# Kernel optimization log

Hardware: AMD Instinct MI355X
Metric: run time of the kernel (lower is better)

Reference implementation:

```python
import math
import jax, jax.numpy as jnp
import numpy as np

WS = 4            # window size
LS = 2 * WS       # local context size
NH = 8            # num heads
DIM = 128
EPS = 1e-5


def setup_inputs() -> dict:
    key = jax.random.key(0)
    ks = jax.random.split(key, 8)
    B, C, H, W = 4, DIM, 48, 48
    features = jax.random.normal(ks[0], (B, C, H, W), dtype=jnp.float32)
    s = 0.02
    return {
        'features': features,
        'ln_w': jnp.ones((C,), jnp.float32),
        'ln_b': jnp.zeros((C,), jnp.float32),
        'q_w': jax.random.normal(ks[1], (C, C), jnp.float32) * s,
        'q_b': jnp.zeros((C,), jnp.float32),
        'kv_w': jax.random.normal(ks[2], (2 * C, C), jnp.float32) * s,
        'kv_b': jnp.zeros((2 * C,), jnp.float32),
        'out_w': jax.random.normal(ks[3], (C, C), jnp.float32) * s,
        'out_b': jnp.zeros((C,), jnp.float32),
    }


def _avgpool_tokens(x, k):
    # x: [B,C,H,W] -> [B, (H//k)*(W//k), C]
    B, C, H, W = x.shape
    t = x.reshape(B, C, H // k, k, W // k, k).mean(axis=(3, 5))
    return t.reshape(B, C, -1).transpose(0, 2, 1)


def reference(features, ln_w, ln_b, q_w, q_b, kv_w, kv_b, out_w, out_b):
    B, C, H, W = features.shape
    Hw, Ww = H // WS, W // WS
    nw = Hw * Ww
    hd = C // NH

    # ---- window partition: [B,C,H,W] -> [B*nw, WS*WS, C]
    qt = features.reshape(B, C, Hw, WS, Ww, WS).transpose(0, 2, 4, 3, 5, 1)
    qt = qt.reshape(B * nw, WS * WS, C)

    # ---- LayerNorm(dim)
    mu = qt.mean(-1, keepdims=True)
    var = qt.var(-1, keepdims=True)
    qt = (qt - mu) / jnp.sqrt(var + EPS) * ln_w + ln_b

    # ---- local context: pad to target, unfold kernel=LS stride=WS
    target = (int(math.sqrt(nw)) - 1) * WS + LS
    ph, pw = max(0, target - H), max(0, target - W)
    pad = ((0, 0), (0, 0), (ph // 2, ph - ph // 2), (pw // 2, pw - pw // 2))
    padded = jnp.pad(features, pad)
    # channel order of patches is (C, kh, kw), same as torch unfold
    patches = jax.lax.conv_general_dilated_patches(
        padded, filter_shape=(LS, LS), window_strides=(WS, WS), padding='VALID')
    local = patches.reshape(B, C, LS * LS, nw).transpose(0, 3, 2, 1)
    local = local.reshape(B * nw, LS * LS, C)

    # ---- multi-scale pooled tokens, broadcast to each window
    mid = _avgpool_tokens(features, 2)      # [B, M, C]
    glo = _avgpool_tokens(features, 4)      # [B, G, C]
    mid = jnp.broadcast_to(mid[:, None], (B, nw) + mid.shape[1:]).reshape(B * nw, -1, C)
    glo = jnp.broadcast_to(glo[:, None], (B, nw) + glo.shape[1:]).reshape(B * nw, -1, C)

    kv_tokens = jnp.concatenate([local, mid, glo], axis=1)  # [B*nw, Nkv, C]

    # ---- projections (torch Linear: x @ W.T + b)
    queries = qt @ q_w.T + q_b
    kv = kv_tokens @ kv_w.T + kv_b
    keys, values = kv[..., :C], kv[..., C:]

    # ---- multi-head attention
    Nq, Nkv = queries.shape[1], keys.shape[1]
    q = queries.reshape(-1, Nq, NH, hd)
    k = keys.reshape(-1, Nkv, NH, hd)
    v = values.reshape(-1, Nkv, NH, hd)
    scores = jnp.einsum('bqhd,bkhd->bhqk', q, k) / math.sqrt(hd)
    weights = jax.nn.softmax(scores, axis=-1)
    attended = jnp.einsum('bhqk,bkhd->bqhd', weights, v).reshape(-1, Nq, C)

    out = attended @ out_w.T + out_b

    # ---- window reconstruction -> [B,C,H,W]
    out = out.reshape(B, Hw, Ww, WS, WS, C).transpose(0, 5, 1, 3, 2, 4)
    out = out.reshape(B, C, H, W)
    return out + features
```

## Files before the change

### kernel.cpp

```cpp
#include <hip/hip_runtime.h>


typedef unsigned short u16;
typedef short v8s __attribute__((ext_vector_type(8)));
typedef v8s __attribute__((may_alias)) v8s_am;
typedef short v4s __attribute__((ext_vector_type(4)));
typedef v4s __attribute__((may_alias)) v4s_am;
typedef float v4f __attribute__((ext_vector_type(4)));

#define MFMA_BF16(a, b, c) __builtin_amdgcn_mfma_f32_16x16x32_bf16(a, b, c, 0, 0, 0)

#if __has_builtin(__builtin_amdgcn_mfma_f32_16x16x16bf16_1k)
#define MFMA16(a, b, c) __builtin_amdgcn_mfma_f32_16x16x16bf16_1k(a, b, c, 0, 0, 0)
#else
static __device__ __forceinline__ v4f mfma16_fb(v4s a, v4s b, v4f c) {
    v8s a8 = {a[0], a[1], a[2], a[3], 0, 0, 0, 0};
    v8s b8 = {b[0], b[1], b[2], b[3], 0, 0, 0, 0};
    return MFMA_BF16(a8, b8, c);
}
#define MFMA16(a, b, c) mfma16_fb(a, b, c)
#endif

#if __has_builtin(__builtin_amdgcn_exp2f)
#define EXP2(x) __builtin_amdgcn_exp2f(x)
#else
#define EXP2(x) exp2f(x)
#endif

__device__ __forceinline__ float b2f(u16 u) {
    union { unsigned int i; float f; } x;
    x.i = ((unsigned int)u) << 16;
    return x.f;
}
__device__ __forceinline__ u16 f2b(float f) {
    union { float f; unsigned int i; } x;
    x.f = f;
    unsigned int u = x.i;
    return (u16)((u + 0x7fffu + ((u >> 16) & 1u)) >> 16);
}

__global__ __launch_bounds__(256) void k_prep(
    const float* __restrict__ F,
    const float* __restrict__ qw, const float* __restrict__ kvw,
    const float* __restrict__ ow,
    const float* __restrict__ lnw, const float* __restrict__ lnb,
    u16* __restrict__ Xt, u16* __restrict__ Wb, float* __restrict__ MuRs,
    u16* __restrict__ Pml)
{
    int blk = blockIdx.x;
    int t = threadIdx.x;
    if (blk >= 304) {
        int gid = (blk - 304) * 256 + t;
        int row = gid >> 4;
        int seg = gid & 15;
        v8s outv;
        if (row < 2304) {
            int b = row / 576, r = row % 576;
            int i = r / 24, j = r % 24;
#pragma unroll
            for (int jc = 0; jc < 8; ++jc) {
                int c = seg * 8 + jc;
                const float* src = F + ((size_t)(b * 128 + c)) * 2304 + (2 * i) * 48 + 2 * j;
                float2 a = *(const float2*)src;
                float2 d = *(const float2*)(src + 48);
                outv[jc] = (short)f2b((a.x + a.y + d.x + d.y) * 0.25f);
            }
        } else {
            int r2 = row - 2304;
            int b = r2 / 144, r = r2 % 144;
            int i = r / 12, j = r % 12;
#pragma unroll
            for (int jc = 0; jc < 8; ++jc) {
                int c = seg * 8 + jc;
                const float* src = F + ((size_t)(b * 128 + c)) * 2304 + (4 * i) * 48 + 4 * j;
                float s = 0.f;
#pragma unroll
                for (int di = 0; di < 4; ++di) {
                    float4 v = *(const float4*)(src + di * 48);
                    s += (v.x + v.y) + (v.z + v.w);
                }
                outv[jc] = (short)f2b(s * 0.0625f);
            }
        }
        *(v8s_am*)&Pml[((size_t)row) * 128 + seg * 8] = outv;
        return;
    }
    if (blk >= 288) {
        int base = (blk - 288) * 4096 + t * 16;
#pragma unroll
        for (int i = 0; i < 4; ++i) {
            int idx = base + i * 4;
            const float* src; int off;
            if (idx < 16384)      { src = qw;  off = idx; }
            else if (idx < 49152) { src = kvw; off = idx - 16384; }
            else                  { src = ow;  off = idx - 49152; }
            float4 v = *(const float4*)(src + off);
            unsigned long long packed =
                (unsigned long long)f2b(v.x) |
                ((unsigned long long)f2b(v.y) << 16) |
                ((unsigned long long)f2b(v.z) << 32) |
                ((unsigned long long)f2b(v.w) << 48);
            *(unsigned long long*)(Wb + idx) = packed;
        }
        if (blk == 288) {
            Wb[65536 + t] = f2b(t < 128 ? lnw[t] : lnb[t - 128]);
        }
        return;
    }
    __shared__ u16 X[128][34];
    int b = blk / 72;
    int p0 = (blk % 72) * 32;
#pragma unroll 4
    for (int i = 0; i < 16; ++i) {
        int c = i * 8 + (t >> 5);
        int pix = t & 31;
        X[c][pix] = f2b(F[((size_t)(b * 128 + c)) * 2304 + p0 + pix]);
    }
    __syncthreads();
    int pix = t >> 3;
    int c0 = (t & 7) * 16;
    size_t row = (size_t)(b * 2304 + p0 + pix) * 128;
    float s = 0.f, s2 = 0.f;
#pragma unroll
    for (int sg = 0; sg < 2; ++sg) {
        v8s raw;
#pragma unroll
        for (int j = 0; j < 8; ++j) {
            u16 u = X[c0 + sg * 8 + j][pix];
            raw[j] = (short)u;
            float v = b2f(u);
            s += v; s2 += v * v;
        }
        *(v8s_am*)&Xt[row + c0 + sg * 8] = raw;
    }
    s += __shfl_xor(s, 1);  s2 += __shfl_xor(s2, 1);
    s += __shfl_xor(s, 2);  s2 += __shfl_xor(s2, 2);
    s += __shfl_xor(s, 4);  s2 += __shfl_xor(s2, 4);
    if ((t & 7) == 0) {
        float mean = s * (1.f / 128.f);
        float var = s2 * (1.f / 128.f) - mean * mean;
        float rstd = rsqrtf(var + 1e-5f);
        MuRs[(b * 2304 + p0 + pix) * 2]     = mean;
        MuRs[(b * 2304 + p0 + pix) * 2 + 1] = rstd;
    }
}

__global__ __launch_bounds__(256) void k_gemm_kv(
    const u16* __restrict__ Pml,
    const u16* __restrict__ W,
    const float* __restrict__ bias,
    u16* __restrict__ KVg,
    u16* __restrict__ VTg)
{
    __shared__ u16 Al[64][136];
    __shared__ u16 Wl[64][136];
    int tm = blockIdx.x * 64, tn = blockIdx.y * 64;
    int t = threadIdx.x;
    {
        int seg = t & 15, r0 = t >> 4;
#pragma unroll
        for (int i = 0; i < 4; ++i) {
            int r = r0 + 16 * i;
            *(v8s_am*)&Al[r][seg * 8] = *(const v8s_am*)&Pml[((size_t)(tm + r)) * 128 + seg * 8];
            *(v8s_am*)&Wl[r][seg * 8] = *(const v8s_am*)&W[((size_t)(tn + r)) * 128 + seg * 8];
        }
    }
    __syncthreads();
    int lane = t & 63, wave = t >> 6;
    int n15 = lane & 15, quad = lane >> 4;
    int wm = (wave & 1) * 32, wn = (wave >> 1) * 32;
    v4f acc[2][2] = {};
#pragma unroll
    for (int kc = 0; kc < 4; ++kc) {
        v8s a[2], bb[2];
#pragma unroll
        for (int im = 0; im < 2; ++im)
            a[im] = *(const v8s_am*)&Al[wm + im * 16 + n15][kc * 32 + quad * 8];
#pragma unroll
        for (int in = 0; in < 2; ++in)
            bb[in] = *(const v8s_am*)&Wl[wn + in * 16 + n15][kc * 32 + quad * 8];
#pragma unroll
        for (int im = 0; im < 2; ++im)
#pragma unroll
            for (int in = 0; in < 2; ++in)
                acc[im][in] = MFMA_BF16(a[im], bb[in], acc[im][in]);
    }
#pragma unroll
    for (int in = 0; in < 2; ++in) {
        int n = tn + wn + in * 16 + n15;
        float bv = bias[n];
#pragma unroll
        for (int im = 0; im < 2; ++im) {
            int mbase = tm + wm + im * 16 + quad * 4;
#pragma unroll
            for (int r = 0; r < 4; ++r) {
                int m = mbase + r;
                u16 h = f2b(acc[im][in][r] + bv);
                if (n < 128) {
                    KVg[((size_t)m) * 128 + n] = h;
                } else {
                    int ch = n - 128, bb2, tok;
                    if (m < 2304) { bb2 = m / 576; tok = m % 576; }
                    else { int r2 = m - 2304; bb2 = r2 / 144; tok = 576 + r2 % 144; }
                    VTg[((size_t)(bb2 * 128 + ch)) * 720 + tok] = h;
                }
            }
        }
    }
}

__global__ __launch_bounds__(512, 4) void k_attn_fused(
    const float* __restrict__ F,
    const u16* __restrict__ Xt,
    const float* __restrict__ MuRs,
    const u16* __restrict__ KVg,
    const u16* __restrict__ VTg,
    const u16* __restrict__ Wb,
    const float* __restrict__ qb,
    const float* __restrict__ kvb,
    const float* __restrict__ ob,
    float* __restrict__ Out)
{
    __shared__ u16 KB[2][64][136];
    __shared__ u16 VtW[8][16][68];

    const u16* qwb  = Wb;
    const u16* kvwb = Wb + 16384;
    const u16* owb  = Wb + 49152;
    const u16* lnwb = Wb + 65536;
    const u16* lnbb = Wb + 65664;
    u16* Atp = &VtW[0][0][0];

    int blk = blockIdx.x;
    int xcd = blk & 7, jj = blk >> 3;
    int b = xcd >> 1;
    int wr = (xcd & 1) * 6 + jj / 12;
    int wc = jj % 12;

    int t = threadIdx.x;
    int lane = t & 63, wave = t >> 6, n15 = lane & 15, quad = lane >> 4;
    v8s zf8 = {};
    v4f zz4 = {0.f, 0.f, 0.f, 0.f};
    const float QSCALE = 0.25f * 1.44269504f;

    int qh = wr * 4 + (n15 >> 2), qw_ = wc * 4 + (n15 & 3);
    int qpix = b * 2304 + qh * 48 + qw_;
    float mu = MuRs[qpix * 2], rstd = MuRs[qpix * 2 + 1];
    v8s xln[4];
#pragma unroll
    for (int kc = 0; kc < 4; ++kc) {
        v8s x  = *(const v8s_am*)&Xt[(size_t)qpix * 128 + kc * 32 + quad * 8];
        v8s lw = *(const v8s_am*)&lnwb[kc * 32 + quad * 8];
        v8s lb = *(const v8s_am*)&lnbb[kc * 32 + quad * 8];
        v8s y;
#pragma unroll
        for (int j = 0; j < 8; ++j)
            y[j] = (short)f2b((b2f((u16)x[j]) - mu) * rstd * b2f((u16)lw[j]) + b2f((u16)lb[j]));
        xln[kc] = y;
    }

    v4s qf;
    {
        int n0 = wave * 16;
        v4f qacc = zz4;
#pragma unroll
        for (int kc = 0; kc < 4; ++kc) {
            v8s aw = *(const v8s_am*)&qwb[((size_t)(n0 + n15)) * 128 + kc * 32 + quad * 8];
            qacc = MFMA_BF16(aw, xln[kc], qacc);
        }
#pragma unroll
        for (int r = 0; r < 4; ++r)
            qf[r] = (short)f2b((qacc[r] + qb[n0 + quad * 4 + r]) * QSCALE);
    }

    v4s kfloc[4];
#pragma unroll
    for (int g = 0; g < 4; ++g) {
        int tl = g * 16 + n15;
        int fh = tl >> 3, fw = tl & 7;
        int hh = wr * 4 - 2 + fh, ww = wc * 4 - 2 + fw;
        bool valid = (hh >= 0 && hh < 48 && ww >= 0 && ww < 48);
        size_t arow = (size_t)(b * 2304 + hh * 48 + ww) * 128;
        v8s xb[4];
#pragma unroll
        for (int kc = 0; kc < 4; ++kc) {
            v8s v = zf8;
            if (valid) v = *(const v8s_am*)&Xt[arow + kc * 32 + quad * 8];
            xb[kc] = v;
        }
#pragma unroll
        for (int s = 0; s < 2; ++s) {
            int sbase = s * 128 + wave * 16;
            v4f acc = zz4;
#pragma unroll
            for (int kc = 0; kc < 4; ++kc) {
                v8s aw = *(const v8s_am*)&kvwb[((size_t)(sbase + n15)) * 128 + kc * 32 + quad * 8];
                acc = MFMA_BF16(aw, xb[kc], acc);
            }
            if (s == 0) {
                v4s k4;
#pragma unroll
                for (int r = 0; r < 4; ++r)
                    k4[r] = (short)f2b(acc[r] + kvb[sbase + quad * 4 + r]);
                kfloc[g] = k4;
            } else {
#pragma unroll
                for (int r = 0; r < 4; ++r)
                    VtW[wave][quad * 4 + r][g * 16 + n15] =
                        f2b(acc[r] + kvb[sbase + quad * 4 + r]);
            }
        }
    }

    v8s stg[2];
#pragma unroll
    for (int i = 0; i < 2; ++i) {
        int chunk = i * 512 + t;
        stg[i] = *(const v8s_am*)&KVg[((size_t)(b * 576 + (chunk >> 4))) * 128 + (chunk & 15) * 8];
    }

    v4f oacc = zz4;
    float ls = 0.f;
    const u16* VTb = VTg + (size_t)b * 92160;

    asm volatile("s_waitcnt lgkmcnt(0)" ::: "memory");
#pragma unroll
    for (int g = 0; g < 4; ++g) {
        v4f St = MFMA16(kfloc[g], qf, zz4);
        float p0 = EXP2(St[0]), p1 = EXP2(St[1]);
        float p2 = EXP2(St[2]), p3 = EXP2(St[3]);
        ls += (p0 + p1) + (p2 + p3);
        v4s pk = {(short)f2b(p0), (short)f2b(p1), (short)f2b(p2), (short)f2b(p3)};
        v4s vf = *(const v4s_am*)&VtW[wave][n15][g * 16 + quad * 4];
        oacc = MFMA16(vf, pk, oacc);
    }

#pragma unroll
    for (int i = 0; i < 2; ++i) {
        int chunk = i * 512 + t;
        *(v8s_am*)&KB[1][chunk >> 4][(chunk & 15) * 8] = stg[i];
    }
    __syncthreads();

    for (int tb = 0; tb <= 10; ++tb) {
        v4s vp[4];
        {
            const u16* vrow = VTb + (size_t)(wave * 16 + n15) * 720 + tb * 64 + quad * 4;
#pragma unroll
            for (int g = 0; g < 4; ++g)
                vp[g] = *(const v4s_am*)(vrow + g * 16);
        }
        int nt_ = tb + 1;
        int rowbase = (nt_ < 9) ? (b * 576 + nt_ * 64)
                                : (2304 + b * 144 + nt_ * 64 - 576);
        int nrows = (nt_ == 11) ? 16 : 64;
        bool sv[2];
#pragma unroll
        for (int i = 0; i < 2; ++i) {
            int chunk = i * 512 + t;
            int rr = chunk >> 4;
            sv[i] = rr < nrows;
            if (sv[i])
                stg[i] = *(const v8s_am*)&KVg[((size_t)(rowbase + rr)) * 128 + (chunk & 15) * 8];
        }
        const u16 (*KBc)[136] = KB[1 - (tb & 1)];
#pragma unroll
        for (int g = 0; g < 4; ++g) {
            v4s kf = *(const v4s_am*)&KBc[g * 16 + n15][wave * 16 + quad * 4];
            v4f St = MFMA16(kf, qf, zz4);
            float p0 = EXP2(St[0]), p1 = EXP2(St[1]);
            float p2 = EXP2(St[2]), p3 = EXP2(St[3]);
            ls += (p0 + p1) + (p2 + p3);
            v4s pk = {(short)f2b(p0), (short)f2b(p1), (short)f2b(p2), (short)f2b(p3)};
            oacc = MFMA16(vp[g], pk, oacc);
        }
#pragma unroll
        for (int i = 0; i < 2; ++i) {
            if (sv[i]) {
                int chunk = i * 512 + t;
                *(v8s_am*)&KB[tb & 1][chunk >> 4][(chunk & 15) * 8] = stg[i];
            }
        }
        __syncthreads();
    }
    {
        v4s vf = *(const v4s_am*)(VTb + (size_t)(wave * 16 + n15) * 720 + 704 + quad * 4);
        v4s kf = *(const v4s_am*)&KB[0][n15][wave * 16 + quad * 4];
        v4f St = MFMA16(kf, qf, zz4);
        float p0 = EXP2(St[0]), p1 = EXP2(St[1]);
        float p2 = EXP2(St[2]), p3 = EXP2(St[3]);
        ls += (p0 + p1) + (p2 + p3);
        v4s pk = {(short)f2b(p0), (short)f2b(p1), (short)f2b(p2), (short)f2b(p3)};
        oacc = MFMA16(vf, pk, oacc);
    }

    ls += __shfl_xor(ls, 16);
    ls += __shfl_xor(ls, 32);
    {
        float inv = 1.f / ls;
        v4s a4 = {(short)f2b(oacc[0] * inv), (short)f2b(oacc[1] * inv),
                  (short)f2b(oacc[2] * inv), (short)f2b(oacc[3] * inv)};
        *(v4s_am*)&Atp[n15 * 136 + wave * 16 + quad * 4] = a4;
    }
    __syncthreads();

    {
        int n0 = wave * 16;
        v4f oa = zz4;
#pragma unroll
        for (int kc = 0; kc < 4; ++kc) {
            v8s af = *(const v8s_am*)&Atp[n15 * 136 + kc * 32 + quad * 8];
            v8s bf = *(const v8s_am*)&owb[((size_t)(n0 + n15)) * 128 + kc * 32 + quad * 8];
            oa = MFMA_BF16(af, bf, oa);
        }
        int c = n0 + n15;
        float bv = ob[c];
#pragma unroll
        for (int r = 0; r < 4; ++r) {
            int pix = quad * 4 + r;
            int hh = wr * 4 + (pix >> 2), ww_ = wc * 4 + (pix & 3);
            size_t idx = ((size_t)(b * 128 + c)) * 2304 + hh * 48 + ww_;
            Out[idx] = oa[r] + bv + F[idx];
        }
    }
}

extern "C" void kernel_launch(void* const* d_in, const int* in_sizes, int n_in,
                              void* d_out, int out_size, void* d_ws, size_t ws_size,
                              hipStream_t stream)
{
    const float* F   = (const float*)d_in[0];
    const float* lnw = (const float*)d_in[1];
    const float* lnb = (const float*)d_in[2];
    const float* qw  = (const float*)d_in[3];
    const float* qb  = (const float*)d_in[4];
    const float* kvw = (const float*)d_in[5];
    const float* kvb = (const float*)d_in[6];
    const float* ow  = (const float*)d_in[7];
    const float* ob  = (const float*)d_in[8];
    float* Out = (float*)d_out;

    u16* ws    = (u16*)d_ws;
    u16* Xt    = ws;
    u16* Pml   = Xt + 9216 * 128;
    u16* KVg   = Pml + 2880 * 128;
    u16* VTg   = KVg + 2880 * 128;
    u16* Wb    = VTg + 4 * 128 * 720;
    float* MuRs = (float*)(Wb + 65792);
    u16* kvwb = Wb + 16384;

    k_prep<<<484, 256, 0, stream>>>(F, qw, kvw, ow, lnw, lnb, Xt, Wb, MuRs, Pml);
    k_gemm_kv<<<dim3(45, 4), 256, 0, stream>>>(Pml, kvwb, kvb, KVg, VTg);
    k_attn_fused<<<576, 512, 0, stream>>>(F, Xt, MuRs, KVg, VTg, Wb,
                                          qb, kvb, ob, Out);
}
```

Before: 135.1 us.

## Process two windows per block and stream head-major K via per-wave LDS

Each attention block now handles two adjacent windows, so the shared pooled K/V tiles loaded from global memory are reused across two query sets, and the grid is halved. K is stored head-major by the KV GEMM, so each wave loads only its own head slice into a private LDS buffer, and the block-wide barrier per tile is removed. V fragments and residual features are prefetched into registers ahead of use. The cost is higher register pressure and less parallelism from the halved grid.

```diff
diff --git a/kernel.cpp b/kernel.cpp
--- a/kernel.cpp
+++ b/kernel.cpp
@@ -149,7 +149,7 @@
     const u16* __restrict__ Pml,
     const u16* __restrict__ W,
     const float* __restrict__ bias,
-    u16* __restrict__ KVg,
+    u16* __restrict__ KVh,
     u16* __restrict__ VTg)
 {
     __shared__ u16 Al[64][136];
@@ -197,7 +197,7 @@
                 int m = mbase + r;
                 u16 h = f2b(acc[im][in][r] + bv);
                 if (n < 128) {
-                    KVg[((size_t)m) * 128 + n] = h;
+                    KVh[((size_t)(n >> 4) * 2880 + m) * 16 + (n & 15)] = h;
                 } else {
                     int ch = n - 128, bb2, tok;
                     if (m < 2304) { bb2 = m / 576; tok = m % 576; }
@@ -213,7 +213,7 @@
     const float* __restrict__ F,
     const u16* __restrict__ Xt,
     const float* __restrict__ MuRs,
-    const u16* __restrict__ KVg,
+    const u16* __restrict__ KVh,
     const u16* __restrict__ VTg,
     const u16* __restrict__ Wb,
     const float* __restrict__ qb,
@@ -221,21 +221,21 @@
     const float* __restrict__ ob,
     float* __restrict__ Out)
 {
-    __shared__ u16 KB[2][64][136];
-    __shared__ u16 VtW[8][16][68];
+    __shared__ u16 KP[8][64][16];
+    __shared__ u16 VtW[8][2][16][68];
 
     const u16* qwb  = Wb;
     const u16* kvwb = Wb + 16384;
     const u16* owb  = Wb + 49152;
     const u16* lnwb = Wb + 65536;
     const u16* lnbb = Wb + 65664;
-    u16* Atp = &VtW[0][0][0];
+    u16* Atp = &VtW[0][0][0][0];
 
     int blk = blockIdx.x;
     int xcd = blk & 7, jj = blk >> 3;
     int b = xcd >> 1;
-    int wr = (xcd & 1) * 6 + jj / 12;
-    int wc = jj % 12;
+    int wr = (xcd & 1) * 6 + jj / 6;
+    int wcp = jj % 6;
 
     int t = threadIdx.x;
     int lane = t & 63, wave = t >> 6, n15 = lane & 15, quad = lane >> 4;
@@ -243,24 +243,39 @@
     v4f zz4 = {0.f, 0.f, 0.f, 0.f};
     const float QSCALE = 0.25f * 1.44269504f;
 
-    int qh = wr * 4 + (n15 >> 2), qw_ = wc * 4 + (n15 & 3);
-    int qpix = b * 2304 + qh * 48 + qw_;
-    float mu = MuRs[qpix * 2], rstd = MuRs[qpix * 2 + 1];
-    v8s xln[4];
-#pragma unroll
-    for (int kc = 0; kc < 4; ++kc) {
-        v8s x  = *(const v8s_am*)&Xt[(size_t)qpix * 128 + kc * 32 + quad * 8];
-        v8s lw = *(const v8s_am*)&lnwb[kc * 32 + quad * 8];
-        v8s lb = *(const v8s_am*)&lnbb[kc * 32 + quad * 8];
-        v8s y;
-#pragma unroll
-        for (int j = 0; j < 8; ++j)
-            y[j] = (short)f2b((b2f((u16)x[j]) - mu) * rstd * b2f((u16)lw[j]) + b2f((u16)lb[j]));
-        xln[kc] = y;
-    }
-
-    v4s qf;
+    u16* KPw = &KP[wave][0][0];
+    const u16* kwave = KVh + (size_t)wave * 46080;
+    const u16* vrow0 = VTg + (size_t)b * 92160
+                     + (size_t)(wave * 16 + n15) * 720 + quad * 4;
+
+    v8s kN0, kN1;
     {
+        const u16* s = kwave + (size_t)(b * 576 + lane) * 16;
+        kN0 = *(const v8s_am*)s; kN1 = *(const v8s_am*)(s + 8);
+    }
+    v4s vpC[4], vpN[4];
+#pragma unroll
+    for (int g = 0; g < 4; ++g) vpC[g] = *(const v4s_am*)(vrow0 + g * 16);
+
+    v4s qf[2];
+#pragma unroll
+    for (int wi = 0; wi < 2; ++wi) {
+        int wc = wcp * 2 + wi;
+        int qh = wr * 4 + (n15 >> 2), qw_ = wc * 4 + (n15 & 3);
+        int qpix = b * 2304 + qh * 48 + qw_;
+        float mu = MuRs[qpix * 2], rstd = MuRs[qpix * 2 + 1];
+        v8s xln[4];
+#pragma unroll
+        for (int kc = 0; kc < 4; ++kc) {
+            v8s x  = *(const v8s_am*)&Xt[(size_t)qpix * 128 + kc * 32 + quad * 8];
+            v8s lw = *(const v8s_am*)&lnwb[kc * 32 + quad * 8];
+            v8s lb = *(const v8s_am*)&lnbb[kc * 32 + quad * 8];
+            v8s y;
+#pragma unroll
+            for (int j = 0; j < 8; ++j)
+                y[j] = (short)f2b((b2f((u16)x[j]) - mu) * rstd * b2f((u16)lw[j]) + b2f((u16)lb[j]));
+            xln[kc] = y;
+        }
         int n0 = wave * 16;
         v4f qacc = zz4;
 #pragma unroll
@@ -268,148 +283,163 @@
             v8s aw = *(const v8s_am*)&qwb[((size_t)(n0 + n15)) * 128 + kc * 32 + quad * 8];
             qacc = MFMA_BF16(aw, xln[kc], qacc);
         }
+        v4s q4;
 #pragma unroll
         for (int r = 0; r < 4; ++r)
-            qf[r] = (short)f2b((qacc[r] + qb[n0 + quad * 4 + r]) * QSCALE);
-    }
-
-    v4s kfloc[4];
-#pragma unroll
-    for (int g = 0; g < 4; ++g) {
-        int tl = g * 16 + n15;
-        int fh = tl >> 3, fw = tl & 7;
-        int hh = wr * 4 - 2 + fh, ww = wc * 4 - 2 + fw;
-        bool valid = (hh >= 0 && hh < 48 && ww >= 0 && ww < 48);
-        size_t arow = (size_t)(b * 2304 + hh * 48 + ww) * 128;
-        v8s xb[4];
-#pragma unroll
-        for (int kc = 0; kc < 4; ++kc) {
-            v8s v = zf8;
-            if (valid) v = *(const v8s_am*)&Xt[arow + kc * 32 + quad * 8];
-            xb[kc] = v;
-        }
-#pragma unroll
-        for (int s = 0; s < 2; ++s) {
-            int sbase = s * 128 + wave * 16;
-            v4f acc = zz4;
+            q4[r] = (short)f2b((qacc[r] + qb[n0 + quad * 4 + r]) * QSCALE);
+        qf[wi] = q4;
+    }
+
+    v4s kfloc[2][4];
+#pragma unroll
+    for (int wi = 0; wi < 2; ++wi) {
+        int wc = wcp * 2 + wi;
+#pragma unroll
+        for (int g = 0; g < 4; ++g) {
+            int tl = g * 16 + n15;
+            int fh = tl >> 3, fw = tl & 7;
+            int hh = wr * 4 - 2 + fh, ww = wc * 4 - 2 + fw;
+            bool valid = (hh >= 0 && hh < 48 && ww >= 0 && ww < 48);
+            size_t arow = (size_t)(b * 2304 + hh * 48 + ww) * 128;
+            v8s xb[4];
 #pragma unroll
             for (int kc = 0; kc < 4; ++kc) {
-                v8s aw = *(const v8s_am*)&kvwb[((size_t)(sbase + n15)) * 128 + kc * 32 + quad * 8];
-                acc = MFMA_BF16(aw, xb[kc], acc);
-            }
-            if (s == 0) {
-                v4s k4;
-#pragma unroll
-                for (int r = 0; r < 4; ++r)
-                    k4[r] = (short)f2b(acc[r] + kvb[sbase + quad * 4 + r]);
-                kfloc[g] = k4;
-            } else {
-#pragma unroll
-                for (int r = 0; r < 4; ++r)
-                    VtW[wave][quad * 4 + r][g * 16 + n15] =
-                        f2b(acc[r] + kvb[sbase + quad * 4 + r]);
-            }
-        }
-    }
-
-    v8s stg[2];
-#pragma unroll
-    for (int i = 0; i < 2; ++i) {
-        int chunk = i * 512 + t;
-        stg[i] = *(const v8s_am*)&KVg[((size_t)(b * 576 + (chunk >> 4))) * 128 + (chunk & 15) * 8];
-    }
-
-    v4f oacc = zz4;
-    float ls = 0.f;
-    const u16* VTb = VTg + (size_t)b * 92160;
+                v8s v = zf8;
+                if (valid) v = *(const v8s_am*)&Xt[arow + kc * 32 + quad * 8];
+                xb[kc] = v;
+            }
+#pragma unroll
+            for (int s = 0; s < 2; ++s) {
+                int sbase = s * 128 + wave * 16;
+                v4f acc = zz4;
+#pragma unroll
+                for (int kc = 0; kc < 4; ++kc) {
+                    v8s aw = *(const v8s_am*)&kvwb[((size_t)(sbase + n15)) * 128 + kc * 32 + quad * 8];
+                    acc = MFMA_BF16(aw, xb[kc], acc);
+                }
+                if (s == 0) {
+                    v4s k4;
+#pragma unroll
+                    for (int r = 0; r < 4; ++r)
+                        k4[r] = (short)f2b(acc[r] + kvb[sbase + quad * 4 + r]);
+                    kfloc[wi][g] = k4;
+                } else {
+#pragma unroll
+                    for (int r = 0; r < 4; ++r)
+                        VtW[wave][wi][quad * 4 + r][g * 16 + n15] =
+                            f2b(acc[r] + kvb[sbase + quad * 4 + r]);
+                }
+            }
+        }
+    }
+
+    v4f oacc[2] = {};
+    float ls0 = 0.f, ls1 = 0.f;
 
     asm volatile("s_waitcnt lgkmcnt(0)" ::: "memory");
 #pragma unroll
-    for (int g = 0; g < 4; ++g) {
-        v4f St = MFMA16(kfloc[g], qf, zz4);
-        float p0 = EXP2(St[0]), p1 = EXP2(St[1]);
-        float p2 = EXP2(St[2]), p3 = EXP2(St[3]);
-        ls += (p0 + p1) + (p2 + p3);
-        v4s pk = {(short)f2b(p0), (short)f2b(p1), (short)f2b(p2), (short)f2b(p3)};
-        v4s vf = *(const v4s_am*)&VtW[wave][n15][g * 16 + quad * 4];
-        oacc = MFMA16(vf, pk, oacc);
-    }
-
-#pragma unroll
-    for (int i = 0; i < 2; ++i) {
-        int chunk = i * 512 + t;
-        *(v8s_am*)&KB[1][chunk >> 4][(chunk & 15) * 8] = stg[i];
-    }
-    __syncthreads();
-
-    for (int tb = 0; tb <= 10; ++tb) {
-        v4s vp[4];
-        {
-            const u16* vrow = VTb + (size_t)(wave * 16 + n15) * 720 + tb * 64 + quad * 4;
-#pragma unroll
-            for (int g = 0; g < 4; ++g)
-                vp[g] = *(const v4s_am*)(vrow + g * 16);
-        }
-        int nt_ = tb + 1;
-        int rowbase = (nt_ < 9) ? (b * 576 + nt_ * 64)
-                                : (2304 + b * 144 + nt_ * 64 - 576);
-        int nrows = (nt_ == 11) ? 16 : 64;
-        bool sv[2];
-#pragma unroll
-        for (int i = 0; i < 2; ++i) {
-            int chunk = i * 512 + t;
-            int rr = chunk >> 4;
-            sv[i] = rr < nrows;
-            if (sv[i])
-                stg[i] = *(const v8s_am*)&KVg[((size_t)(rowbase + rr)) * 128 + (chunk & 15) * 8];
-        }
-        const u16 (*KBc)[136] = KB[1 - (tb & 1)];
+    for (int wi = 0; wi < 2; ++wi) {
 #pragma unroll
         for (int g = 0; g < 4; ++g) {
-            v4s kf = *(const v4s_am*)&KBc[g * 16 + n15][wave * 16 + quad * 4];
-            v4f St = MFMA16(kf, qf, zz4);
+            v4f St = MFMA16(kfloc[wi][g], qf[wi], zz4);
             float p0 = EXP2(St[0]), p1 = EXP2(St[1]);
             float p2 = EXP2(St[2]), p3 = EXP2(St[3]);
-            ls += (p0 + p1) + (p2 + p3);
+            if (wi == 0) ls0 += (p0 + p1) + (p2 + p3);
+            else         ls1 += (p0 + p1) + (p2 + p3);
             v4s pk = {(short)f2b(p0), (short)f2b(p1), (short)f2b(p2), (short)f2b(p3)};
-            oacc = MFMA16(vp[g], pk, oacc);
-        }
-#pragma unroll
-        for (int i = 0; i < 2; ++i) {
-            if (sv[i]) {
-                int chunk = i * 512 + t;
-                *(v8s_am*)&KB[tb & 1][chunk >> 4][(chunk & 15) * 8] = stg[i];
-            }
-        }
-        __syncthreads();
-    }
+            v4s vf = *(const v4s_am*)&VtW[wave][wi][n15][g * 16 + quad * 4];
+            oacc[wi] = MFMA16(vf, pk, oacc[wi]);
+        }
+    }
+    __syncthreads();
+
+    float fres[2][4];
+#pragma unroll
+    for (int wi = 0; wi < 2; ++wi) {
+        int wc = wcp * 2 + wi;
+        int c = wave * 16 + n15;
+#pragma unroll
+        for (int r = 0; r < 4; ++r) {
+            int pix = quad * 4 + r;
+            int hh = wr * 4 + (pix >> 2), ww_ = wc * 4 + (pix & 3);
+            fres[wi][r] = F[((size_t)(b * 128 + c)) * 2304 + hh * 48 + ww_];
+        }
+    }
+
+    *(v8s_am*)&KPw[lane * 16]     = kN0;
+    *(v8s_am*)&KPw[lane * 16 + 8] = kN1;
     {
-        v4s vf = *(const v4s_am*)(VTb + (size_t)(wave * 16 + n15) * 720 + 704 + quad * 4);
-        v4s kf = *(const v4s_am*)&KB[0][n15][wave * 16 + quad * 4];
-        v4f St = MFMA16(kf, qf, zz4);
-        float p0 = EXP2(St[0]), p1 = EXP2(St[1]);
-        float p2 = EXP2(St[2]), p3 = EXP2(St[3]);
-        ls += (p0 + p1) + (p2 + p3);
-        v4s pk = {(short)f2b(p0), (short)f2b(p1), (short)f2b(p2), (short)f2b(p3)};
-        oacc = MFMA16(vf, pk, oacc);
-    }
-
-    ls += __shfl_xor(ls, 16);
-    ls += __shfl_xor(ls, 32);
-    {
+        const u16* s = kwave + (size_t)(b * 576 + 64 + lane) * 16;
+        kN0 = *(const v8s_am*)s; kN1 = *(const v8s_am*)(s + 8);
+    }
+#pragma unroll
+    for (int g = 0; g < 4; ++g) vpN[g] = *(const v4s_am*)(vrow0 + 64 + g * 16);
+
+#pragma unroll
+    for (int tb = 0; tb <= 11; ++tb) {
+        v4s kf[4];
+#pragma unroll
+        for (int g = 0; g < 4; ++g)
+            kf[g] = *(const v4s_am*)&KPw[(g * 16 + n15) * 16 + quad * 4];
+        if (tb < 11) {
+            *(v8s_am*)&KPw[lane * 16]     = kN0;
+            *(v8s_am*)&KPw[lane * 16 + 8] = kN1;
+            if (tb < 10) {
+                int t2 = tb + 2;
+                int row = (t2 < 9) ? (b * 576 + t2 * 64 + lane)
+                                   : (2304 + b * 144 + (t2 - 9) * 64 + lane);
+                if (t2 == 11) row = min(2304 + b * 144 + 128 + lane, 2879);
+                const u16* s = kwave + (size_t)row * 16;
+                kN0 = *(const v8s_am*)s; kN1 = *(const v8s_am*)(s + 8);
+            }
+        }
+#pragma unroll
+        for (int g = 0; g < ((tb == 11) ? 1 : 4); ++g) {
+            v4f St0 = MFMA16(kf[g], qf[0], zz4);
+            v4f St1 = MFMA16(kf[g], qf[1], zz4);
+            float a0 = EXP2(St0[0]), a1 = EXP2(St0[1]), a2 = EXP2(St0[2]), a3 = EXP2(St0[3]);
+            float b0 = EXP2(St1[0]), b1 = EXP2(St1[1]), b2 = EXP2(St1[2]), b3 = EXP2(St1[3]);
+            ls0 += (a0 + a1) + (a2 + a3);
+            ls1 += (b0 + b1) + (b2 + b3);
+            v4s pk0 = {(short)f2b(a0), (short)f2b(a1), (short)f2b(a2), (short)f2b(a3)};
+            v4s pk1 = {(short)f2b(b0), (short)f2b(b1), (short)f2b(b2), (short)f2b(b3)};
+            oacc[0] = MFMA16(vpC[g], pk0, oacc[0]);
+            oacc[1] = MFMA16(vpC[g], pk1, oacc[1]);
+        }
+        if (tb < 11) {
+#pragma unroll
+            for (int g = 0; g < 4; ++g) vpC[g] = vpN[g];
+            if (tb < 10) {
+                int t2 = tb + 2;
+#pragma unroll
+                for (int g = 0; g < 4; ++g) {
+                    int off = (t2 == 11) ? 704 : (t2 * 64 + g * 16);
+                    vpN[g] = *(const v4s_am*)(vrow0 + off);
+                }
+            }
+        }
+    }
+
+#pragma unroll
+    for (int wi = 0; wi < 2; ++wi) {
+        float ls = wi == 0 ? ls0 : ls1;
+        ls += __shfl_xor(ls, 16);
+        ls += __shfl_xor(ls, 32);
         float inv = 1.f / ls;
-        v4s a4 = {(short)f2b(oacc[0] * inv), (short)f2b(oacc[1] * inv),
-                  (short)f2b(oacc[2] * inv), (short)f2b(oacc[3] * inv)};
-        *(v4s_am*)&Atp[n15 * 136 + wave * 16 + quad * 4] = a4;
+        v4s a4 = {(short)f2b(oacc[wi][0] * inv), (short)f2b(oacc[wi][1] * inv),
+                  (short)f2b(oacc[wi][2] * inv), (short)f2b(oacc[wi][3] * inv)};
+        *(v4s_am*)&Atp[wi * 2176 + n15 * 136 + wave * 16 + quad * 4] = a4;
     }
     __syncthreads();
 
-    {
+#pragma unroll
+    for (int wi = 0; wi < 2; ++wi) {
+        int wc = wcp * 2 + wi;
         int n0 = wave * 16;
         v4f oa = zz4;
 #pragma unroll
         for (int kc = 0; kc < 4; ++kc) {
-            v8s af = *(const v8s_am*)&Atp[n15 * 136 + kc * 32 + quad * 8];
+            v8s af = *(const v8s_am*)&Atp[wi * 2176 + n15 * 136 + kc * 32 + quad * 8];
             v8s bf = *(const v8s_am*)&owb[((size_t)(n0 + n15)) * 128 + kc * 32 + quad * 8];
             oa = MFMA_BF16(af, bf, oa);
         }
@@ -420,7 +450,7 @@
             int pix = quad * 4 + r;
             int hh = wr * 4 + (pix >> 2), ww_ = wc * 4 + (pix & 3);
             size_t idx = ((size_t)(b * 128 + c)) * 2304 + hh * 48 + ww_;
-            Out[idx] = oa[r] + bv + F[idx];
+            Out[idx] = oa[r] + bv + fres[wi][r];
         }
     }
 }
@@ -443,14 +473,14 @@
     u16* ws    = (u16*)d_ws;
     u16* Xt    = ws;
     u16* Pml   = Xt + 9216 * 128;
-    u16* KVg   = Pml + 2880 * 128;
-    u16* VTg   = KVg + 2880 * 128;
+    u16* KVh   = Pml + 2880 * 128;
+    u16* VTg   = KVh + 8 * 2880 * 16;
     u16* Wb    = VTg + 4 * 128 * 720;
     float* MuRs = (float*)(Wb + 65792);
     u16* kvwb = Wb + 16384;
 
     k_prep<<<484, 256, 0, stream>>>(F, qw, kvw, ow, lnw, lnb, Xt, Wb, MuRs, Pml);
-    k_gemm_kv<<<dim3(45, 4), 256, 0, stream>>>(Pml, kvwb, kvb, KVg, VTg);
-    k_attn_fused<<<576, 512, 0, stream>>>(F, Xt, MuRs, KVg, VTg, Wb,
+    k_gemm_kv<<<dim3(45, 4), 256, 0, stream>>>(Pml, kvwb, kvb, KVh, VTg);
+    k_attn_fused<<<288, 512, 0, stream>>>(F, Xt, MuRs, KVh, VTg, Wb,
                                           qb, kvb, ob, Out);
 }
```

Result: slower. 191.9 us (+42.0%).

## Store keys head-major and stage per-wave to drop block barriers in attention loop

Applied to the files above, without the earlier changes.

The KV GEMM now writes keys in a head-major layout ([head][token][16]), so each wave loads only its own head's key slice into a private LDS buffer. This removes the block-wide double-buffered key tile and the __syncthreads in each of the 11 loop iterations, since waves now only touch their own data. Loads are software-pipelined two tiles ahead through registers. Launch bounds drop from 4 to 2 waves per EU, which frees registers but may lower occupancy. Each wave's 64-lane, 32-byte-per-lane global loads may be less coalesced than the old layout.

```diff
diff --git a/kernel.cpp b/kernel.cpp
--- a/kernel.cpp
+++ b/kernel.cpp
@@ -149,7 +149,7 @@
     const u16* __restrict__ Pml,
     const u16* __restrict__ W,
     const float* __restrict__ bias,
-    u16* __restrict__ KVg,
+    u16* __restrict__ KVh,
     u16* __restrict__ VTg)
 {
     __shared__ u16 Al[64][136];
@@ -197,7 +197,7 @@
                 int m = mbase + r;
                 u16 h = f2b(acc[im][in][r] + bv);
                 if (n < 128) {
-                    KVg[((size_t)m) * 128 + n] = h;
+                    KVh[((size_t)(n >> 4) * 2880 + m) * 16 + (n & 15)] = h;
                 } else {
                     int ch = n - 128, bb2, tok;
                     if (m < 2304) { bb2 = m / 576; tok = m % 576; }
@@ -209,11 +209,11 @@
     }
 }
 
-__global__ __launch_bounds__(512, 4) void k_attn_fused(
+__global__ __launch_bounds__(512, 2) void k_attn_fused(
     const float* __restrict__ F,
     const u16* __restrict__ Xt,
     const float* __restrict__ MuRs,
-    const u16* __restrict__ KVg,
+    const u16* __restrict__ KVh,
     const u16* __restrict__ VTg,
     const u16* __restrict__ Wb,
     const float* __restrict__ qb,
@@ -221,7 +221,7 @@
     const float* __restrict__ ob,
     float* __restrict__ Out)
 {
-    __shared__ u16 KB[2][64][136];
+    __shared__ u16 KP[8][64][16];
     __shared__ u16 VtW[8][16][68];
 
     const u16* qwb  = Wb;
@@ -242,6 +242,17 @@
     v8s zf8 = {};
     v4f zz4 = {0.f, 0.f, 0.f, 0.f};
     const float QSCALE = 0.25f * 1.44269504f;
+
+    u16* KPw = &KP[wave][0][0];
+    const u16* kwave = KVh + (size_t)wave * 46080;
+    const u16* vrow0 = VTg + (size_t)b * 92160
+                     + (size_t)(wave * 16 + n15) * 720 + quad * 4;
+
+    v8s kN0, kN1;
+    {
+        const u16* s = kwave + (size_t)(b * 576 + lane) * 16;
+        kN0 = *(const v8s_am*)s; kN1 = *(const v8s_am*)(s + 8);
+    }
 
     int qh = wr * 4 + (n15 >> 2), qw_ = wc * 4 + (n15 & 3);
     int qpix = b * 2304 + qh * 48 + qw_;
@@ -312,16 +323,8 @@
         }
     }
 
-    v8s stg[2];
-#pragma unroll
-    for (int i = 0; i < 2; ++i) {
-        int chunk = i * 512 + t;
-        stg[i] = *(const v8s_am*)&KVg[((size_t)(b * 576 + (chunk >> 4))) * 128 + (chunk & 15) * 8];
-    }
-
     v4f oacc = zz4;
     float ls = 0.f;
-    const u16* VTb = VTg + (size_t)b * 92160;
 
     asm volatile("s_waitcnt lgkmcnt(0)" ::: "memory");
 #pragma unroll
@@ -334,58 +337,47 @@
         v4s vf = *(const v4s_am*)&VtW[wave][n15][g * 16 + quad * 4];
         oacc = MFMA16(vf, pk, oacc);
     }
-
-#pragma unroll
-    for (int i = 0; i < 2; ++i) {
-        int chunk = i * 512 + t;
-        *(v8s_am*)&KB[1][chunk >> 4][(chunk & 15) * 8] = stg[i];
-    }
     __syncthreads();
 
+    *(v8s_am*)&KPw[lane * 16]     = kN0;
+    *(v8s_am*)&KPw[lane * 16 + 8] = kN1;
+    {
+        const u16* s = kwave + (size_t)(b * 576 + 64 + lane) * 16;
+        kN0 = *(const v8s_am*)s; kN1 = *(const v8s_am*)(s + 8);
+    }
+
     for (int tb = 0; tb <= 10; ++tb) {
+        v4s kf[4];
+#pragma unroll
+        for (int g = 0; g < 4; ++g)
+            kf[g] = *(const v4s_am*)&KPw[(g * 16 + n15) * 16 + quad * 4];
+        *(v8s_am*)&KPw[lane * 16]     = kN0;
+        *(v8s_am*)&KPw[lane * 16 + 8] = kN1;
+        if (tb < 10) {
+            int t2 = tb + 2;
+            int row = (t2 < 9) ? (b * 576 + t2 * 64 + lane)
+                               : (2304 + b * 144 + (t2 - 9) * 64 + lane);
+            if (t2 == 11) row = 2304 + b * 144 + 128 + n15;
+            const u16* s = kwave + (size_t)row * 16;
+            kN0 = *(const v8s_am*)s; kN1 = *(const v8s_am*)(s + 8);
+        }
         v4s vp[4];
-        {
-            const u16* vrow = VTb + (size_t)(wave * 16 + n15) * 720 + tb * 64 + quad * 4;
-#pragma unroll
-            for (int g = 0; g < 4; ++g)
-                vp[g] = *(const v4s_am*)(vrow + g * 16);
-        }
-        int nt_ = tb + 1;
-        int rowbase = (nt_ < 9) ? (b * 576 + nt_ * 64)
-                                : (2304 + b * 144 + nt_ * 64 - 576);
-        int nrows = (nt_ == 11) ? 16 : 64;
-        bool sv[2];
-#pragma unroll
-        for (int i = 0; i < 2; ++i) {
-            int chunk = i * 512 + t;
-            int rr = chunk >> 4;
-            sv[i] = rr < nrows;
-            if (sv[i])
-                stg[i] = *(const v8s_am*)&KVg[((size_t)(rowbase + rr)) * 128 + (chunk & 15) * 8];
-        }
-        const u16 (*KBc)[136] = KB[1 - (tb & 1)];
+#pragma unroll
+        for (int g = 0; g < 4; ++g)
+            vp[g] = *(const v4s_am*)(vrow0 + tb * 64 + g * 16);
 #pragma unroll
         for (int g = 0; g < 4; ++g) {
-            v4s kf = *(const v4s_am*)&KBc[g * 16 + n15][wave * 16 + quad * 4];
-            v4f St = MFMA16(kf, qf, zz4);
+            v4f St = MFMA16(kf[g], qf, zz4);
             float p0 = EXP2(St[0]), p1 = EXP2(St[1]);
             float p2 = EXP2(St[2]), p3 = EXP2(St[3]);
             ls += (p0 + p1) + (p2 + p3);
             v4s pk = {(short)f2b(p0), (short)f2b(p1), (short)f2b(p2), (short)f2b(p3)};
             oacc = MFMA16(vp[g], pk, oacc);
         }
-#pragma unroll
-        for (int i = 0; i < 2; ++i) {
-            if (sv[i]) {
-                int chunk = i * 512 + t;
-                *(v8s_am*)&KB[tb & 1][chunk >> 4][(chunk & 15) * 8] = stg[i];
-            }
-        }
-        __syncthreads();
-    }
-    {
-        v4s vf = *(const v4s_am*)(VTb + (size_t)(wave * 16 + n15) * 720 + 704 + quad * 4);
-        v4s kf = *(const v4s_am*)&KB[0][n15][wave * 16 + quad * 4];
+    }
+    {
+        v4s kf = *(const v4s_am*)&KPw[n15 * 16 + quad * 4];
+        v4s vf = *(const v4s_am*)(vrow0 + 704);
         v4f St = MFMA16(kf, qf, zz4);
         float p0 = EXP2(St[0]), p1 = EXP2(St[1]);
         float p2 = EXP2(St[2]), p3 = EXP2(St[3]);
@@ -443,14 +435,14 @@
     u16* ws    = (u16*)d_ws;
     u16* Xt    = ws;
     u16* Pml   = Xt + 9216 * 128;
-    u16* KVg   = Pml + 2880 * 128;
-    u16* VTg   = KVg + 2880 * 128;
+    u16* KVh   = Pml + 2880 * 128;
+    u16* VTg   = KVh + 8 * 2880 * 16;
     u16* Wb    = VTg + 4 * 128 * 720;
     float* MuRs = (float*)(Wb + 65792);
     u16* kvwb = Wb + 16384;
 
     k_prep<<<484, 256, 0, stream>>>(F, qw, kvw, ow, lnw, lnb, Xt, Wb, MuRs, Pml);
-    k_gemm_kv<<<dim3(45, 4), 256, 0, stream>>>(Pml, kvwb, kvb, KVg, VTg);
-    k_attn_fused<<<576, 512, 0, stream>>>(F, Xt, MuRs, KVg, VTg, Wb,
+    k_gemm_kv<<<dim3(45, 4), 256, 0, stream>>>(Pml, kvwb, kvb, KVh, VTg);
+    k_attn_fused<<<576, 512, 0, stream>>>(F, Xt, MuRs, KVh, VTg, Wb,
                                           qb, kvb, ob, Out);
 }
```

Measured after the change: 129.1 us. 4.5% less time.
